# Kernel tuning notes

Hardware: AMD Instinct MI355X
Metric: run time of the kernel (lower is better)

Reference implementation:

```python
import jax, jax.numpy as jnp
import numpy as np

B, CIN, COUT, T, H, W = 8, 512, 256, 8, 16, 16


def conv1x1(x, w, b):
    # 1x1x1 Conv3d == per-position channel GEMM. x:[B,Ci,T,H,W], w:[Co,Ci], b:[Co]
    return jnp.einsum('bcthw,oc->bothw', x, w) + b[None, :, None, None, None]


def setup_inputs() -> dict:
    key = jax.random.key(0)
    ks = jax.random.split(key, 12)
    s_in = 1.0 / np.sqrt(CIN)
    s_out = 1.0 / np.sqrt(COUT)
    return {
        'x': jax.random.normal(ks[0], (B, CIN, T, H, W), jnp.float32),
        'query': jax.random.normal(ks[1], (B, CIN, T, H, W), jnp.float32),
        'key_w': jax.random.uniform(ks[2], (COUT, CIN), jnp.float32, -s_in, s_in),
        'key_b': jax.random.uniform(ks[3], (COUT,), jnp.float32, -s_in, s_in),
        'val_w': jax.random.uniform(ks[4], (COUT, CIN), jnp.float32, -s_in, s_in),
        'val_b': jax.random.uniform(ks[5], (COUT,), jnp.float32, -s_in, s_in),
        'query_w': jax.random.uniform(ks[6], (COUT, CIN), jnp.float32, -s_in, s_in),
        'query_b': jax.random.uniform(ks[7], (COUT,), jnp.float32, -s_in, s_in),
        'up_w': jax.random.uniform(ks[8], (CIN, COUT), jnp.float32, -s_out, s_out),
        'up_b': jax.random.uniform(ks[9], (CIN,), jnp.float32, -s_out, s_out),
        'scaling': jnp.asarray(1.0, jnp.float32),
    }


def reference(x, query, key_w, key_b, val_w, val_b, query_w, query_b, up_w, up_b, scaling):
    b, ci, t, h, w = x.shape
    n = t * h * w
    co = key_w.shape[0]
    k = conv1x1(x, key_w, key_b).reshape(b, co, n)          # [B,Co,N]
    q = conv1x1(query, query_w, query_b).reshape(b, co, n)  # [B,Co,N]
    v = conv1x1(x, val_w, val_b).reshape(b, co, n)          # [B,Co,N]
    # attention = (key^T @ query) / sqrt(Co)  -> [B,N,N], softmax over last dim
    attn = jnp.einsum('bcn,bcm->bnm', k, q) / jnp.sqrt(jnp.asarray(co, x.dtype))
    attn = jax.nn.softmax(attn, axis=-1)
    out = jnp.einsum('bnm,bcm->bnc', attn, v)               # [B,N,Co]
    # faithful to torch .view: raw-memory reshape of [B,N,Co] -> [B,Co,T,H,W]
    out = out.reshape(b, co, t, h, w)
    out = conv1x1(out, up_w, up_b)                          # [B,Ci,T,H,W]
    return x + out * scaling
```

## Files before the change

kernel.cpp:

```cpp
#include <hip/hip_runtime.h>
#include <hip/hip_fp8.h>
#include <math.h>

#define NB 8
#define CI 512
#define CO 256
#define NN 2048
#define SCALE 0.0625f
#define SPLIT 4

typedef __bf16 v8bf __attribute__((ext_vector_type(8)));
typedef __bf16 v4bf __attribute__((ext_vector_type(4)));
typedef float  f32x4  __attribute__((ext_vector_type(4)));
typedef float  f32x16 __attribute__((ext_vector_type(16)));
typedef unsigned char u8;
typedef long i64t;

static __device__ __forceinline__ u8 to_fp8(float x) {
    __hip_fp8_e4m3 t(x);
    return (u8)t.__x;
}

static __device__ __forceinline__ i64t pack64(unsigned lo, unsigned hi) {
    return (i64t)(((unsigned long long)hi << 32) | (unsigned long long)lo);
}

__global__ __launch_bounds__(256, 2)
void proj3_kernel(const float* __restrict__ x, const float* __restrict__ query,
                  const float* __restrict__ wk, const float* __restrict__ bk,
                  const float* __restrict__ wv, const float* __restrict__ bv,
                  const float* __restrict__ wq, const float* __restrict__ bq,
                  u8* __restrict__ outK, u8* __restrict__ outV, u8* __restrict__ outQ)
{
    const int b = blockIdx.z, n0 = blockIdx.x * 128, co0 = blockIdx.y * 64;
    const int tid = threadIdx.x;
    const int wave = tid >> 6, lane = tid & 63;
    const int l16 = lane & 15, quad = lane >> 4;
    const int wn = wave & 1, wc = wave >> 1;

    __shared__ __bf16 Xt[128][40];
    __shared__ __bf16 Qt[128][40];
    __shared__ __bf16 Wks[64][40];
    __shared__ __bf16 Wvs[64][40];
    __shared__ __bf16 Wqs[64][40];

    const float* xb = x + (size_t)b * CI * NN;
    const float* qb = query + (size_t)b * CI * NN;

    f32x4 acck[4][2], accv[2][4], accq[4][2];
    #pragma unroll
    for (int i = 0; i < 4; ++i)
        #pragma unroll
        for (int j = 0; j < 2; ++j) {
            acck[i][j] = f32x4{0,0,0,0}; accv[j][i] = f32x4{0,0,0,0};
            accq[i][j] = f32x4{0,0,0,0};
        }

    const int xn = tid & 127;
    const int xc = tid >> 7;

    for (int k0 = 0; k0 < CI; k0 += 32) {
        #pragma unroll
        for (int g = 0; g < 2; ++g) {
            int cg = xc + g * 2;
            v8bf z, w;
            #pragma unroll
            for (int j = 0; j < 8; ++j) {
                z[j] = (__bf16)xb[(size_t)(k0 + cg * 8 + j) * NN + n0 + xn];
                w[j] = (__bf16)qb[(size_t)(k0 + cg * 8 + j) * NN + n0 + xn];
            }
            *(v8bf*)&Xt[xn][cg * 8] = z;
            *(v8bf*)&Qt[xn][cg * 8] = w;
        }
        #pragma unroll
        for (int g = 0; g < 2; ++g) {
            int f = tid + 256 * g;
            int co = f >> 3, cq = f & 7;
            float4 a = *(const float4*)(wk + (size_t)(co0 + co) * CI + k0 + cq * 4);
            float4 c = *(const float4*)(wv + (size_t)(co0 + co) * CI + k0 + cq * 4);
            float4 d = *(const float4*)(wq + (size_t)(co0 + co) * CI + k0 + cq * 4);
            *(v4bf*)&Wks[co][cq * 4] = v4bf{(__bf16)a.x, (__bf16)a.y, (__bf16)a.z, (__bf16)a.w};
            *(v4bf*)&Wvs[co][cq * 4] = v4bf{(__bf16)c.x, (__bf16)c.y, (__bf16)c.z, (__bf16)c.w};
            *(v4bf*)&Wqs[co][cq * 4] = v4bf{(__bf16)d.x, (__bf16)d.y, (__bf16)d.z, (__bf16)d.w};
        }
        __syncthreads();
        v8bf ax[4], aqx[4], bkf[2], bqf[2];
        #pragma unroll
        for (int i = 0; i < 4; ++i) {
            ax[i]  = *(const v8bf*)&Xt[wn * 64 + i * 16 + l16][quad * 8];
            aqx[i] = *(const v8bf*)&Qt[wn * 64 + i * 16 + l16][quad * 8];
        }
        #pragma unroll
        for (int j = 0; j < 2; ++j) {
            bkf[j] = *(const v8bf*)&Wks[wc * 32 + j * 16 + l16][quad * 8];
            bqf[j] = *(const v8bf*)&Wqs[wc * 32 + j * 16 + l16][quad * 8];
        }
        #pragma unroll
        for (int i = 0; i < 4; ++i)
            #pragma unroll
            for (int j = 0; j < 2; ++j) {
                acck[i][j] = __builtin_amdgcn_mfma_f32_16x16x32_bf16(ax[i],  bkf[j], acck[i][j], 0, 0, 0);
                accq[i][j] = __builtin_amdgcn_mfma_f32_16x16x32_bf16(aqx[i], bqf[j], accq[i][j], 0, 0, 0);
            }
        {
            v8bf avf[2];
            #pragma unroll
            for (int j = 0; j < 2; ++j) avf[j] = *(const v8bf*)&Wvs[wc * 32 + j * 16 + l16][quad * 8];
            #pragma unroll
            for (int j = 0; j < 2; ++j)
                #pragma unroll
                for (int i = 0; i < 4; ++i)
                    accv[j][i] = __builtin_amdgcn_mfma_f32_16x16x32_bf16(avf[j], ax[i], accv[j][i], 0, 0, 0);
        }
        __syncthreads();
    }
    #pragma unroll
    for (int i = 0; i < 4; ++i) {
        int n = n0 + wn * 64 + i * 16 + quad * 4;
        #pragma unroll
        for (int j = 0; j < 2; ++j) {
            int co = co0 + wc * 32 + j * 16 + l16;
            float bkk = bk[co], bqq = bq[co];
            u8* dk = outK + ((size_t)b * NN + n) * CO + co;
            u8* dq = outQ + ((size_t)b * NN + n) * CO + co;
            #pragma unroll
            for (int r = 0; r < 4; ++r) {
                dk[(size_t)r * CO] = to_fp8(acck[i][j][r] + bkk);
                dq[(size_t)r * CO] = to_fp8(accq[i][j][r] + bqq);
            }
        }
    }
    #pragma unroll
    for (int j = 0; j < 2; ++j) {
        int co = co0 + wc * 32 + j * 16 + quad * 4;
        #pragma unroll
        for (int r = 0; r < 4; ++r) {
            float bvv = bv[co + r];
            #pragma unroll
            for (int i = 0; i < 4; ++i) {
                int n = n0 + wn * 64 + i * 16 + l16;
                outV[((size_t)b * CO + co + r) * NN + n] = to_fp8(accv[j][i][r] + bvv);
            }
        }
    }
}

__global__ __launch_bounds__(256, 2)
void attn_kernel(const u8* __restrict__ kT, const u8* __restrict__ qT,
                 const u8* __restrict__ vT2, __bf16* __restrict__ Opart,
                 float* __restrict__ lbuf)
{
    const int b = blockIdx.z, part = blockIdx.y, n0 = blockIdx.x * 128;
    const int tid = threadIdx.x;
    const int wave = tid >> 6, lane = tid & 63;
    const int l32 = lane & 31, hs = lane >> 5;

    __shared__ i64t Ks8[64][33];
    __shared__ i64t Vt8[256][9];

    const int start = part * (NN / SPLIT);
    const u8* Ksrc = qT + ((size_t)b * NN + start) * CO;
    const u8* Vsrc = vT2 + (size_t)b * CO * NN + start;

    i64t aq[16];
    {
        const u8* qrow = kT + ((size_t)b * NN + n0 + wave * 32 + l32) * CO + hs * 8;
        #pragma unroll
        for (int s = 0; s < 16; ++s) aq[s] = *(const i64t*)(qrow + s * 16);
    }

    f32x16 acc[8];
    #pragma unroll
    for (int t = 0; t < 8; ++t)
        #pragma unroll
        for (int r = 0; r < 16; ++r) acc[t][r] = 0.f;
    float lp = 0.f;

    int4 kx[4], vx[4];
    #pragma unroll
    for (int r2 = 0; r2 < 4; ++r2) {
        int c = tid + 256 * r2;
        kx[r2] = *(const int4*)(Ksrc + (size_t)(c >> 4) * CO + (c & 15) * 16);
        vx[r2] = *(const int4*)(Vsrc + (size_t)(c >> 2) * NN + (c & 3) * 16);
    }

    for (int it = 0; it < NN / SPLIT / 64; ++it) {
        #pragma unroll
        for (int r2 = 0; r2 < 4; ++r2) {
            int c = tid + 256 * r2;
            i64t* kd = &Ks8[c >> 4][(c & 15) * 2];
            kd[0] = *(const i64t*)&kx[r2].x;
            kd[1] = *(const i64t*)&kx[r2].z;
            i64t* vd = &Vt8[c >> 2][(c & 3) * 2];
            vd[0] = pack64((unsigned)vx[r2].x, (unsigned)vx[r2].z);
            vd[1] = pack64((unsigned)vx[r2].y, (unsigned)vx[r2].w);
        }
        __syncthreads();

        if (it + 1 < NN / SPLIT / 64) {
            const u8* Kit = Ksrc + (size_t)(it + 1) * 64 * CO;
            const u8* Vit = Vsrc + (it + 1) * 64;
            #pragma unroll
            for (int r2 = 0; r2 < 4; ++r2) {
                int c = tid + 256 * r2;
                kx[r2] = *(const int4*)(Kit + (size_t)(c >> 4) * CO + (c & 15) * 16);
                vx[r2] = *(const int4*)(Vit + (size_t)(c >> 2) * NN + (c & 3) * 16);
            }
        }

        int dpk[8];
        #pragma unroll
        for (int sub = 0; sub < 2; ++sub) {
            f32x16 sacc;
            #pragma unroll
            for (int r = 0; r < 16; ++r) sacc[r] = 0.f;
            __builtin_amdgcn_s_setprio(1);
            #pragma unroll
            for (int s = 0; s < 16; ++s) {
                i64t kf = Ks8[sub * 32 + l32][s * 2 + hs];
                sacc = __builtin_amdgcn_mfma_f32_32x32x16_fp8_fp8(kf, aq[s], sacc, 0, 0, 0);
            }
            __builtin_amdgcn_s_setprio(0);
            #pragma unroll
            for (int r = 0; r < 16; ++r) {
                sacc[r] = __expf(sacc[r] * SCALE);
                lp += sacc[r];
            }
            #pragma unroll
            for (int g = 0; g < 4; ++g) {
                int lo = __builtin_amdgcn_cvt_pk_fp8_f32(sacc[4*g+0], sacc[4*g+1], 0, false);
                dpk[sub * 4 + g] = __builtin_amdgcn_cvt_pk_fp8_f32(sacc[4*g+2], sacc[4*g+3], lo, true);
            }
        }
        i64t pa[4];
        #pragma unroll
        for (int c = 0; c < 4; ++c)
            pa[c] = pack64((unsigned)dpk[2 * c], (unsigned)dpk[2 * c + 1]);

        __builtin_amdgcn_s_setprio(1);
        #pragma unroll
        for (int t = 0; t < 8; ++t) {
            #pragma unroll
            for (int c = 0; c < 4; ++c) {
                i64t bvf = Vt8[t * 32 + l32][c * 2 + hs];
                acc[t] = __builtin_amdgcn_mfma_f32_32x32x16_fp8_fp8(pa[c], bvf, acc[t], 0, 0, 0);
            }
        }
        __builtin_amdgcn_s_setprio(0);
        __syncthreads();
    }

    lp += __shfl_xor(lp, 32);
    if (hs == 0)
        lbuf[(size_t)(part * NB + b) * NN + n0 + wave * 32 + l32] = lp;

    const size_t qbase = (size_t)(part * NB + b) * NN + n0 + wave * 32;
    #pragma unroll
    for (int t = 0; t < 8; ++t)
        #pragma unroll
        for (int r = 0; r < 16; ++r) {
            int row = (r & 3) + 8 * (r >> 2) + 4 * hs;
            Opart[(qbase + row) * CO + t * 32 + l32] = (__bf16)acc[t][r];
        }
}

__global__ __launch_bounds__(256)
void merge_kernel(const __bf16* __restrict__ Opart, const float* __restrict__ lbuf,
                  __bf16* __restrict__ ob)
{
    int gid = blockIdx.x * 256 + threadIdx.x;
    int chunk = gid & 31;
    int row = gid >> 5;
    float ls = 0.f;
    #pragma unroll
    for (int p = 0; p < SPLIT; ++p) ls += lbuf[(size_t)p * NB * NN + row];
    float inv = 1.0f / ls;
    float o[8] = {0,0,0,0,0,0,0,0};
    #pragma unroll
    for (int p = 0; p < SPLIT; ++p) {
        v8bf v = *(const v8bf*)(Opart + ((size_t)p * NB * NN + row) * CO + chunk * 8);
        #pragma unroll
        for (int j = 0; j < 8; ++j) o[j] += (float)v[j];
    }
    v8bf res;
    #pragma unroll
    for (int j = 0; j < 8; ++j) res[j] = (__bf16)(o[j] * inv);
    *(v8bf*)(ob + (size_t)row * CO + chunk * 8) = res;
}

__global__ __launch_bounds__(256)
void up_kernel(const __bf16* __restrict__ ob, const float* __restrict__ x,
               const float* __restrict__ w2, const float* __restrict__ b2,
               const float* __restrict__ scaling, float* __restrict__ out)
{
    const int b = blockIdx.z, n0 = blockIdx.x * 128, ci0 = blockIdx.y * 128;
    const int tid = threadIdx.x;
    const int wave = tid >> 6, lane = tid & 63;
    const int l16 = lane & 15, quad = lane >> 4;
    const int wn = wave & 1, wci = wave >> 1;

    __shared__ __bf16 Zt[128][40];
    __shared__ __bf16 Wt[128][40];

    const __bf16* obb = ob + (size_t)b * CO * NN;

    f32x4 acc[4][4];
    #pragma unroll
    for (int i = 0; i < 4; ++i)
        #pragma unroll
        for (int j = 0; j < 4; ++j) acc[i][j] = f32x4{0,0,0,0};

    const int zn = tid & 127, zc = tid >> 7;

    for (int k0 = 0; k0 < CO; k0 += 32) {
        #pragma unroll
        for (int g = 0; g < 2; ++g) {
            int cg = zc + g * 2;
            v8bf z;
            #pragma unroll
            for (int j = 0; j < 8; ++j)
                z[j] = obb[(size_t)(k0 + cg * 8 + j) * NN + n0 + zn];
            *(v8bf*)&Zt[zn][cg * 8] = z;
        }
        #pragma unroll
        for (int g = 0; g < 4; ++g) {
            int f = tid + 256 * g;
            int ci = f >> 3, cq = f & 7;
            float4 v = *(const float4*)(w2 + (size_t)(ci0 + ci) * CO + k0 + cq * 4);
            *(v4bf*)&Wt[ci][cq * 4] = v4bf{(__bf16)v.x, (__bf16)v.y, (__bf16)v.z, (__bf16)v.w};
        }
        __syncthreads();
        v8bf aw[4], bz[4];
        #pragma unroll
        for (int i = 0; i < 4; ++i) aw[i] = *(const v8bf*)&Wt[wci * 64 + i * 16 + l16][quad * 8];
        #pragma unroll
        for (int j = 0; j < 4; ++j) bz[j] = *(const v8bf*)&Zt[wn * 64 + j * 16 + l16][quad * 8];
        #pragma unroll
        for (int i = 0; i < 4; ++i)
            #pragma unroll
            for (int j = 0; j < 4; ++j)
                acc[i][j] = __builtin_amdgcn_mfma_f32_16x16x32_bf16(aw[i], bz[j], acc[i][j], 0, 0, 0);
        __syncthreads();
    }
    float sc = scaling[0];
    #pragma unroll
    for (int i = 0; i < 4; ++i) {
        int ci = ci0 + wci * 64 + i * 16 + quad * 4;
        #pragma unroll
        for (int r = 0; r < 4; ++r) {
            float bvv = b2[ci + r];
            #pragma unroll
            for (int j = 0; j < 4; ++j) {
                int n = n0 + wn * 64 + j * 16 + l16;
                size_t gi = ((size_t)b * CI + ci + r) * NN + n;
                out[gi] = x[gi] + sc * (acc[i][j][r] + bvv);
            }
        }
    }
}

extern "C" void kernel_launch(void* const* d_in, const int* in_sizes, int n_in,
                              void* d_out, int out_size, void* d_ws, size_t ws_size,
                              hipStream_t stream)
{
    (void)in_sizes; (void)n_in; (void)out_size; (void)ws_size;
    const float* x       = (const float*)d_in[0];
    const float* query   = (const float*)d_in[1];
    const float* key_w   = (const float*)d_in[2];
    const float* key_b   = (const float*)d_in[3];
    const float* val_w   = (const float*)d_in[4];
    const float* val_b   = (const float*)d_in[5];
    const float* query_w = (const float*)d_in[6];
    const float* query_b = (const float*)d_in[7];
    const float* up_w    = (const float*)d_in[8];
    const float* up_b    = (const float*)d_in[9];
    const float* scaling = (const float*)d_in[10];
    float* out = (float*)d_out;

    const size_t TEN = (size_t)NB * NN * CO;
    u8* kT  = (u8*)d_ws;
    u8* qT  = kT + TEN;
    u8* vT2 = qT + TEN;
    __bf16* ob    = (__bf16*)(vT2 + TEN);
    __bf16* Opart = ob + TEN;
    float*  lbuf  = (float*)(Opart + (size_t)SPLIT * TEN);

    dim3 blk(256);
    proj3_kernel<<<dim3(NN / 128, CO / 64, NB), blk, 0, stream>>>(
        x, query, key_w, key_b, val_w, val_b, query_w, query_b, kT, vT2, qT);
    attn_kernel<<<dim3(NN / 128, SPLIT, NB), blk, 0, stream>>>(kT, qT, vT2, Opart, lbuf);
    merge_kernel<<<dim3((NB * NN * CO / 8) / 256), blk, 0, stream>>>(Opart, lbuf, ob);
    up_kernel<<<dim3(NN / 128, CI / 128, NB), blk, 0, stream>>>(ob, x, up_w, up_b, scaling, out);
}
```

Baseline: 206.9 us.

## Halve projection N-tile and register-prefetch next K slice of inputs and weights

```diff
diff --git a/kernel.cpp b/kernel.cpp
--- a/kernel.cpp
+++ b/kernel.cpp
@@ -25,98 +25,112 @@
     return (i64t)(((unsigned long long)hi << 32) | (unsigned long long)lo);
 }
 
-__global__ __launch_bounds__(256, 2)
+__global__ __launch_bounds__(256, 3)
 void proj3_kernel(const float* __restrict__ x, const float* __restrict__ query,
                   const float* __restrict__ wk, const float* __restrict__ bk,
                   const float* __restrict__ wv, const float* __restrict__ bv,
                   const float* __restrict__ wq, const float* __restrict__ bq,
                   u8* __restrict__ outK, u8* __restrict__ outV, u8* __restrict__ outQ)
 {
-    const int b = blockIdx.z, n0 = blockIdx.x * 128, co0 = blockIdx.y * 64;
+    const int b = blockIdx.z, n0 = blockIdx.x * 64, co0 = blockIdx.y * 64;
     const int tid = threadIdx.x;
     const int wave = tid >> 6, lane = tid & 63;
     const int l16 = lane & 15, quad = lane >> 4;
     const int wn = wave & 1, wc = wave >> 1;
 
-    __shared__ __bf16 Xt[128][40];
-    __shared__ __bf16 Qt[128][40];
+    __shared__ __bf16 Xt[64][40];
+    __shared__ __bf16 Qt[64][40];
     __shared__ __bf16 Wks[64][40];
     __shared__ __bf16 Wvs[64][40];
     __shared__ __bf16 Wqs[64][40];
 
-    const float* xb = x + (size_t)b * CI * NN;
-    const float* qb = query + (size_t)b * CI * NN;
-
-    f32x4 acck[4][2], accv[2][4], accq[4][2];
-    #pragma unroll
-    for (int i = 0; i < 4; ++i)
+    const int xn = tid & 63;
+    const int xc = tid >> 6;
+    const float* xp = x     + (size_t)b * CI * NN + (size_t)xc * 8 * NN + n0 + xn;
+    const float* qp = query + (size_t)b * CI * NN + (size_t)xc * 8 * NN + n0 + xn;
+
+    const int wco0 = tid >> 3, wcq = tid & 7;
+    const int wco1 = (tid + 256) >> 3, wcq1 = tid & 7;
+    const float* wkp0 = wk + (size_t)(co0 + wco0) * CI + wcq * 4;
+    const float* wvp0 = wv + (size_t)(co0 + wco0) * CI + wcq * 4;
+    const float* wqp0 = wq + (size_t)(co0 + wco0) * CI + wcq * 4;
+    const float* wkp1 = wk + (size_t)(co0 + wco1) * CI + wcq1 * 4;
+    const float* wvp1 = wv + (size_t)(co0 + wco1) * CI + wcq1 * 4;
+    const float* wqp1 = wq + (size_t)(co0 + wco1) * CI + wcq1 * 4;
+
+    f32x4 acck[2][2], accv[2][2], accq[2][2];
+    #pragma unroll
+    for (int i = 0; i < 2; ++i)
         #pragma unroll
         for (int j = 0; j < 2; ++j) {
             acck[i][j] = f32x4{0,0,0,0}; accv[j][i] = f32x4{0,0,0,0};
             accq[i][j] = f32x4{0,0,0,0};
         }
 
-    const int xn = tid & 127;
-    const int xc = tid >> 7;
+    float xz[8], qz[8];
+    float4 wkf[2], wvf[2], wqf[2];
+    #pragma unroll
+    for (int j = 0; j < 8; ++j) { xz[j] = xp[(size_t)j * NN]; qz[j] = qp[(size_t)j * NN]; }
+    wkf[0] = *(const float4*)(wkp0); wvf[0] = *(const float4*)(wvp0); wqf[0] = *(const float4*)(wqp0);
+    wkf[1] = *(const float4*)(wkp1); wvf[1] = *(const float4*)(wvp1); wqf[1] = *(const float4*)(wqp1);
 
     for (int k0 = 0; k0 < CI; k0 += 32) {
-        #pragma unroll
-        for (int g = 0; g < 2; ++g) {
-            int cg = xc + g * 2;
+        {
             v8bf z, w;
             #pragma unroll
+            for (int j = 0; j < 8; ++j) { z[j] = (__bf16)xz[j]; w[j] = (__bf16)qz[j]; }
+            *(v8bf*)&Xt[xn][xc * 8] = z;
+            *(v8bf*)&Qt[xn][xc * 8] = w;
+            *(v4bf*)&Wks[wco0][wcq * 4]  = v4bf{(__bf16)wkf[0].x, (__bf16)wkf[0].y, (__bf16)wkf[0].z, (__bf16)wkf[0].w};
+            *(v4bf*)&Wvs[wco0][wcq * 4]  = v4bf{(__bf16)wvf[0].x, (__bf16)wvf[0].y, (__bf16)wvf[0].z, (__bf16)wvf[0].w};
+            *(v4bf*)&Wqs[wco0][wcq * 4]  = v4bf{(__bf16)wqf[0].x, (__bf16)wqf[0].y, (__bf16)wqf[0].z, (__bf16)wqf[0].w};
+            *(v4bf*)&Wks[wco1][wcq1 * 4] = v4bf{(__bf16)wkf[1].x, (__bf16)wkf[1].y, (__bf16)wkf[1].z, (__bf16)wkf[1].w};
+            *(v4bf*)&Wvs[wco1][wcq1 * 4] = v4bf{(__bf16)wvf[1].x, (__bf16)wvf[1].y, (__bf16)wvf[1].z, (__bf16)wvf[1].w};
+            *(v4bf*)&Wqs[wco1][wcq1 * 4] = v4bf{(__bf16)wqf[1].x, (__bf16)wqf[1].y, (__bf16)wqf[1].z, (__bf16)wqf[1].w};
+        }
+        __syncthreads();
+
+        if (k0 + 32 < CI) {
+            const size_t koff = (size_t)(k0 + 32) * NN;
+            #pragma unroll
             for (int j = 0; j < 8; ++j) {
-                z[j] = (__bf16)xb[(size_t)(k0 + cg * 8 + j) * NN + n0 + xn];
-                w[j] = (__bf16)qb[(size_t)(k0 + cg * 8 + j) * NN + n0 + xn];
-            }
-            *(v8bf*)&Xt[xn][cg * 8] = z;
-            *(v8bf*)&Qt[xn][cg * 8] = w;
-        }
-        #pragma unroll
-        for (int g = 0; g < 2; ++g) {
-            int f = tid + 256 * g;
-            int co = f >> 3, cq = f & 7;
-            float4 a = *(const float4*)(wk + (size_t)(co0 + co) * CI + k0 + cq * 4);
-            float4 c = *(const float4*)(wv + (size_t)(co0 + co) * CI + k0 + cq * 4);
-            float4 d = *(const float4*)(wq + (size_t)(co0 + co) * CI + k0 + cq * 4);
-            *(v4bf*)&Wks[co][cq * 4] = v4bf{(__bf16)a.x, (__bf16)a.y, (__bf16)a.z, (__bf16)a.w};
-            *(v4bf*)&Wvs[co][cq * 4] = v4bf{(__bf16)c.x, (__bf16)c.y, (__bf16)c.z, (__bf16)c.w};
-            *(v4bf*)&Wqs[co][cq * 4] = v4bf{(__bf16)d.x, (__bf16)d.y, (__bf16)d.z, (__bf16)d.w};
-        }
-        __syncthreads();
-        v8bf ax[4], aqx[4], bkf[2], bqf[2];
-        #pragma unroll
-        for (int i = 0; i < 4; ++i) {
-            ax[i]  = *(const v8bf*)&Xt[wn * 64 + i * 16 + l16][quad * 8];
-            aqx[i] = *(const v8bf*)&Qt[wn * 64 + i * 16 + l16][quad * 8];
+                xz[j] = xp[koff + (size_t)j * NN];
+                qz[j] = qp[koff + (size_t)j * NN];
+            }
+            wkf[0] = *(const float4*)(wkp0 + k0 + 32); wvf[0] = *(const float4*)(wvp0 + k0 + 32);
+            wqf[0] = *(const float4*)(wqp0 + k0 + 32);
+            wkf[1] = *(const float4*)(wkp1 + k0 + 32); wvf[1] = *(const float4*)(wvp1 + k0 + 32);
+            wqf[1] = *(const float4*)(wqp1 + k0 + 32);
+        }
+
+        v8bf ax[2], aqx[2], bkf[2], bqf[2], bvf[2];
+        #pragma unroll
+        for (int i = 0; i < 2; ++i) {
+            ax[i]  = *(const v8bf*)&Xt[wn * 32 + i * 16 + l16][quad * 8];
+            aqx[i] = *(const v8bf*)&Qt[wn * 32 + i * 16 + l16][quad * 8];
         }
         #pragma unroll
         for (int j = 0; j < 2; ++j) {
             bkf[j] = *(const v8bf*)&Wks[wc * 32 + j * 16 + l16][quad * 8];
             bqf[j] = *(const v8bf*)&Wqs[wc * 32 + j * 16 + l16][quad * 8];
-        }
-        #pragma unroll
-        for (int i = 0; i < 4; ++i)
+            bvf[j] = *(const v8bf*)&Wvs[wc * 32 + j * 16 + l16][quad * 8];
+        }
+        __builtin_amdgcn_s_setprio(1);
+        #pragma unroll
+        for (int i = 0; i < 2; ++i)
             #pragma unroll
             for (int j = 0; j < 2; ++j) {
                 acck[i][j] = __builtin_amdgcn_mfma_f32_16x16x32_bf16(ax[i],  bkf[j], acck[i][j], 0, 0, 0);
                 accq[i][j] = __builtin_amdgcn_mfma_f32_16x16x32_bf16(aqx[i], bqf[j], accq[i][j], 0, 0, 0);
-            }
-        {
-            v8bf avf[2];
-            #pragma unroll
-            for (int j = 0; j < 2; ++j) avf[j] = *(const v8bf*)&Wvs[wc * 32 + j * 16 + l16][quad * 8];
-            #pragma unroll
-            for (int j = 0; j < 2; ++j)
-                #pragma unroll
-                for (int i = 0; i < 4; ++i)
-                    accv[j][i] = __builtin_amdgcn_mfma_f32_16x16x32_bf16(avf[j], ax[i], accv[j][i], 0, 0, 0);
-        }
-        __syncthreads();
-    }
-    #pragma unroll
-    for (int i = 0; i < 4; ++i) {
-        int n = n0 + wn * 64 + i * 16 + quad * 4;
+                accv[j][i] = __builtin_amdgcn_mfma_f32_16x16x32_bf16(bvf[j], ax[i],  accv[j][i], 0, 0, 0);
+            }
+        __builtin_amdgcn_s_setprio(0);
+        __syncthreads();
+    }
+
+    #pragma unroll
+    for (int i = 0; i < 2; ++i) {
+        int n = n0 + wn * 32 + i * 16 + quad * 4;
         #pragma unroll
         for (int j = 0; j < 2; ++j) {
             int co = co0 + wc * 32 + j * 16 + l16;
@@ -137,8 +151,8 @@
         for (int r = 0; r < 4; ++r) {
             float bvv = bv[co + r];
             #pragma unroll
-            for (int i = 0; i < 4; ++i) {
-                int n = n0 + wn * 64 + i * 16 + l16;
+            for (int i = 0; i < 2; ++i) {
+                int n = n0 + wn * 32 + i * 16 + l16;
                 outV[((size_t)b * CO + co + r) * NN + n] = to_fp8(accv[j][i][r] + bvv);
             }
         }
@@ -386,7 +400,7 @@
     float*  lbuf  = (float*)(Opart + (size_t)SPLIT * TEN);
 
     dim3 blk(256);
-    proj3_kernel<<<dim3(NN / 128, CO / 64, NB), blk, 0, stream>>>(
+    proj3_kernel<<<dim3(NN / 64, CO / 64, NB), blk, 0, stream>>>(
         x, query, key_w, key_b, val_w, val_b, query_w, query_b, kT, vT2, qT);
     attn_kernel<<<dim3(NN / 128, SPLIT, NB), blk, 0, stream>>>(kT, qT, vT2, Opart, lbuf);
     merge_kernel<<<dim3((NB * NN * CO / 8) / 256), blk, 0, stream>>>(Opart, lbuf, ob);
```

Result: slower. 229.3 us (+10.8%).

## Prefetch next K-slice into registers and swizzle LDS tiles in projection kernel

Applied to the files above, without the earlier changes.

```diff
diff --git a/kernel.cpp b/kernel.cpp
--- a/kernel.cpp
+++ b/kernel.cpp
@@ -44,8 +44,20 @@
     __shared__ __bf16 Wvs[64][40];
     __shared__ __bf16 Wqs[64][40];
 
-    const float* xb = x + (size_t)b * CI * NN;
-    const float* qb = query + (size_t)b * CI * NN;
+    const int xn = tid & 127;
+    const int xc = tid >> 7;
+    const int xsw = (xn >> 3) & 3;
+    const float* xp = x     + (size_t)b * CI * NN + n0 + xn;
+    const float* qp = query + (size_t)b * CI * NN + n0 + xn;
+
+    const int wco0 = tid >> 3, wcq = tid & 7;
+    const int wco1 = wco0 + 32;
+    const float* wkp0 = wk + (size_t)(co0 + wco0) * CI + wcq * 4;
+    const float* wvp0 = wv + (size_t)(co0 + wco0) * CI + wcq * 4;
+    const float* wqp0 = wq + (size_t)(co0 + wco0) * CI + wcq * 4;
+    const float* wkp1 = wk + (size_t)(co0 + wco1) * CI + wcq * 4;
+    const float* wvp1 = wv + (size_t)(co0 + wco1) * CI + wcq * 4;
+    const float* wqp1 = wq + (size_t)(co0 + wco1) * CI + wcq * 4;
 
     f32x4 acck[4][2], accv[2][4], accq[4][2];
     #pragma unroll
@@ -56,45 +68,71 @@
             accq[i][j] = f32x4{0,0,0,0};
         }
 
-    const int xn = tid & 127;
-    const int xc = tid >> 7;
+    float xz[2][8], qz[2][8];
+    float4 wkf[2], wvf[2], wqf[2];
+    #pragma unroll
+    for (int g = 0; g < 2; ++g) {
+        const int cg = xc + g * 2;
+        #pragma unroll
+        for (int j = 0; j < 8; ++j) {
+            xz[g][j] = xp[(size_t)(cg * 8 + j) * NN];
+            qz[g][j] = qp[(size_t)(cg * 8 + j) * NN];
+        }
+    }
+    wkf[0] = *(const float4*)(wkp0); wvf[0] = *(const float4*)(wvp0); wqf[0] = *(const float4*)(wqp0);
+    wkf[1] = *(const float4*)(wkp1); wvf[1] = *(const float4*)(wvp1); wqf[1] = *(const float4*)(wqp1);
 
     for (int k0 = 0; k0 < CI; k0 += 32) {
         #pragma unroll
         for (int g = 0; g < 2; ++g) {
-            int cg = xc + g * 2;
+            const int cg = xc + g * 2;
+            const int col = (cg ^ xsw) * 8;
             v8bf z, w;
             #pragma unroll
-            for (int j = 0; j < 8; ++j) {
-                z[j] = (__bf16)xb[(size_t)(k0 + cg * 8 + j) * NN + n0 + xn];
-                w[j] = (__bf16)qb[(size_t)(k0 + cg * 8 + j) * NN + n0 + xn];
-            }
-            *(v8bf*)&Xt[xn][cg * 8] = z;
-            *(v8bf*)&Qt[xn][cg * 8] = w;
-        }
-        #pragma unroll
-        for (int g = 0; g < 2; ++g) {
-            int f = tid + 256 * g;
-            int co = f >> 3, cq = f & 7;
-            float4 a = *(const float4*)(wk + (size_t)(co0 + co) * CI + k0 + cq * 4);
-            float4 c = *(const float4*)(wv + (size_t)(co0 + co) * CI + k0 + cq * 4);
-            float4 d = *(const float4*)(wq + (size_t)(co0 + co) * CI + k0 + cq * 4);
-            *(v4bf*)&Wks[co][cq * 4] = v4bf{(__bf16)a.x, (__bf16)a.y, (__bf16)a.z, (__bf16)a.w};
-            *(v4bf*)&Wvs[co][cq * 4] = v4bf{(__bf16)c.x, (__bf16)c.y, (__bf16)c.z, (__bf16)c.w};
-            *(v4bf*)&Wqs[co][cq * 4] = v4bf{(__bf16)d.x, (__bf16)d.y, (__bf16)d.z, (__bf16)d.w};
-        }
-        __syncthreads();
-        v8bf ax[4], aqx[4], bkf[2], bqf[2];
+            for (int j = 0; j < 8; ++j) { z[j] = (__bf16)xz[g][j]; w[j] = (__bf16)qz[g][j]; }
+            *(v8bf*)&Xt[xn][col] = z;
+            *(v8bf*)&Qt[xn][col] = w;
+        }
+        *(v4bf*)&Wks[wco0][wcq * 4] = v4bf{(__bf16)wkf[0].x, (__bf16)wkf[0].y, (__bf16)wkf[0].z, (__bf16)wkf[0].w};
+        *(v4bf*)&Wvs[wco0][wcq * 4] = v4bf{(__bf16)wvf[0].x, (__bf16)wvf[0].y, (__bf16)wvf[0].z, (__bf16)wvf[0].w};
+        *(v4bf*)&Wqs[wco0][wcq * 4] = v4bf{(__bf16)wqf[0].x, (__bf16)wqf[0].y, (__bf16)wqf[0].z, (__bf16)wqf[0].w};
+        *(v4bf*)&Wks[wco1][wcq * 4] = v4bf{(__bf16)wkf[1].x, (__bf16)wkf[1].y, (__bf16)wkf[1].z, (__bf16)wkf[1].w};
+        *(v4bf*)&Wvs[wco1][wcq * 4] = v4bf{(__bf16)wvf[1].x, (__bf16)wvf[1].y, (__bf16)wvf[1].z, (__bf16)wvf[1].w};
+        *(v4bf*)&Wqs[wco1][wcq * 4] = v4bf{(__bf16)wqf[1].x, (__bf16)wqf[1].y, (__bf16)wqf[1].z, (__bf16)wqf[1].w};
+        __syncthreads();
+
+        if (k0 + 32 < CI) {
+            const size_t koff = (size_t)(k0 + 32) * NN;
+            #pragma unroll
+            for (int g = 0; g < 2; ++g) {
+                const int cg = xc + g * 2;
+                #pragma unroll
+                for (int j = 0; j < 8; ++j) {
+                    xz[g][j] = xp[koff + (size_t)(cg * 8 + j) * NN];
+                    qz[g][j] = qp[koff + (size_t)(cg * 8 + j) * NN];
+                }
+            }
+            wkf[0] = *(const float4*)(wkp0 + k0 + 32); wvf[0] = *(const float4*)(wvp0 + k0 + 32);
+            wqf[0] = *(const float4*)(wqp0 + k0 + 32);
+            wkf[1] = *(const float4*)(wkp1 + k0 + 32); wvf[1] = *(const float4*)(wvp1 + k0 + 32);
+            wqf[1] = *(const float4*)(wqp1 + k0 + 32);
+        }
+
+        v8bf ax[4], aqx[4], bkf[2], bqf[2], bvf2[2];
         #pragma unroll
         for (int i = 0; i < 4; ++i) {
-            ax[i]  = *(const v8bf*)&Xt[wn * 64 + i * 16 + l16][quad * 8];
-            aqx[i] = *(const v8bf*)&Qt[wn * 64 + i * 16 + l16][quad * 8];
+            const int row = wn * 64 + i * 16 + l16;
+            const int col = (quad ^ ((row >> 3) & 3)) * 8;
+            ax[i]  = *(const v8bf*)&Xt[row][col];
+            aqx[i] = *(const v8bf*)&Qt[row][col];
         }
         #pragma unroll
         for (int j = 0; j < 2; ++j) {
-            bkf[j] = *(const v8bf*)&Wks[wc * 32 + j * 16 + l16][quad * 8];
-            bqf[j] = *(const v8bf*)&Wqs[wc * 32 + j * 16 + l16][quad * 8];
-        }
+            bkf[j]  = *(const v8bf*)&Wks[wc * 32 + j * 16 + l16][quad * 8];
+            bqf[j]  = *(const v8bf*)&Wqs[wc * 32 + j * 16 + l16][quad * 8];
+            bvf2[j] = *(const v8bf*)&Wvs[wc * 32 + j * 16 + l16][quad * 8];
+        }
+        __builtin_amdgcn_s_setprio(1);
         #pragma unroll
         for (int i = 0; i < 4; ++i)
             #pragma unroll
@@ -102,18 +140,15 @@
                 acck[i][j] = __builtin_amdgcn_mfma_f32_16x16x32_bf16(ax[i],  bkf[j], acck[i][j], 0, 0, 0);
                 accq[i][j] = __builtin_amdgcn_mfma_f32_16x16x32_bf16(aqx[i], bqf[j], accq[i][j], 0, 0, 0);
             }
-        {
-            v8bf avf[2];
-            #pragma unroll
-            for (int j = 0; j < 2; ++j) avf[j] = *(const v8bf*)&Wvs[wc * 32 + j * 16 + l16][quad * 8];
-            #pragma unroll
-            for (int j = 0; j < 2; ++j)
-                #pragma unroll
-                for (int i = 0; i < 4; ++i)
-                    accv[j][i] = __builtin_amdgcn_mfma_f32_16x16x32_bf16(avf[j], ax[i], accv[j][i], 0, 0, 0);
-        }
-        __syncthreads();
-    }
+        #pragma unroll
+        for (int j = 0; j < 2; ++j)
+            #pragma unroll
+            for (int i = 0; i < 4; ++i)
+                accv[j][i] = __builtin_amdgcn_mfma_f32_16x16x32_bf16(bvf2[j], ax[i], accv[j][i], 0, 0, 0);
+        __builtin_amdgcn_s_setprio(0);
+        __syncthreads();
+    }
+
     #pragma unroll
     for (int i = 0; i < 4; ++i) {
         int n = n0 + wn * 64 + i * 16 + quad * 4;
```

Result: slower. 217.1 us (+4.9%).
